# Optimization experiments

Measured on AMD Instinct MI355X. Metric: run time of the kernel, lower is better.

## Reference

```python
import jax, jax.numpy as jnp
import numpy as np

H = 4096
B = 64


def _lstm_cell(x, h, c, W_ih, W_hh, b_ih, b_hh):
    # PyTorch gate order: i, f, g, o. gates: [B, 4H]
    gates = x @ W_ih.T + b_ih + h @ W_hh.T + b_hh
    i, f, g, o = jnp.split(gates, 4, axis=-1)
    c_new = jax.nn.sigmoid(f) * c + jax.nn.sigmoid(i) * jnp.tanh(g)
    h_new = jax.nn.sigmoid(o) * jnp.tanh(c_new)
    return h_new, c_new


def setup_inputs() -> dict:
    key = jax.random.key(0)
    ks = jax.random.split(key, 16)
    s = 0.02
    inp = {
        "current_features": jax.random.normal(ks[0], (B, H), jnp.float32),
        "h0": jax.random.normal(ks[1], (2, B, H), jnp.float32),
        "c0": jax.random.normal(ks[2], (2, B, H), jnp.float32),
        # LSTM layer 0
        "W_ih0": jax.random.normal(ks[3], (4 * H, H), jnp.float32) * s,
        "W_hh0": jax.random.normal(ks[4], (4 * H, H), jnp.float32) * s,
        "b_ih0": jax.random.normal(ks[5], (4 * H,), jnp.float32) * s,
        "b_hh0": jax.random.normal(ks[6], (4 * H,), jnp.float32) * s,
        # LSTM layer 1
        "W_ih1": jax.random.normal(ks[7], (4 * H, H), jnp.float32) * s,
        "W_hh1": jax.random.normal(ks[8], (4 * H, H), jnp.float32) * s,
        "b_ih1": jax.random.normal(ks[9], (4 * H,), jnp.float32) * s,
        "b_hh1": jax.random.normal(ks[10], (4 * H,), jnp.float32) * s,
        # count estimator head
        "Wc1": jax.random.normal(ks[11], (H // 2, H), jnp.float32) * s,
        "bc1": jax.random.normal(ks[12], (H // 2,), jnp.float32) * s,
        "Wc2": jax.random.normal(ks[13], (1, H // 2), jnp.float32) * s,
        "bc2": jax.random.normal(ks[14], (1,), jnp.float32) * s,
    }
    return inp


def reference(current_features, h0, c0,
              W_ih0, W_hh0, b_ih0, b_hh0,
              W_ih1, W_hh1, b_ih1, b_hh1,
              Wc1, bc1, Wc2, bc2):
    # Single-step 2-layer LSTM (seq_len=1; inter-layer dropout inactive in eval)
    h1, c1 = _lstm_cell(current_features, h0[0], c0[0], W_ih0, W_hh0, b_ih0, b_hh0)
    h2, c2 = _lstm_cell(h1, h0[1], c0[1], W_ih1, W_hh1, b_ih1, b_hh1)
    memory_state = h2  # [B, H]
    h_new = jnp.stack([h1, h2], axis=0)  # [2, B, H]
    c_new = jnp.stack([c1, c2], axis=0)
    # count head: Linear -> ReLU -> Linear -> ReLU
    hid = jax.nn.relu(memory_state @ Wc1.T + bc1)
    count_estimate = jax.nn.relu(hid @ Wc2.T + bc2)  # [B, 1]
    return memory_state, (h_new, c_new), count_estimate
```

## Files before the change

kernel.cpp:

```cpp
#include <hip/hip_runtime.h>

#define HD 4096
#define NB 64

typedef __attribute__((ext_vector_type(4))) float f32x4;
typedef __attribute__((ext_vector_type(8))) short bf16x8;
typedef __attribute__((ext_vector_type(4))) short s16x4;

__device__ __forceinline__ short f2bf(float f) {
    unsigned u = __float_as_uint(f);
    u += 0x7fffu + ((u >> 16) & 1u);
    return (short)(u >> 16);
}

__device__ __forceinline__ bf16x8 cvt8(f32x4 lo, f32x4 hi) {
    bf16x8 r;
    r[0] = f2bf(lo[0]); r[1] = f2bf(lo[1]); r[2] = f2bf(lo[2]); r[3] = f2bf(lo[3]);
    r[4] = f2bf(hi[0]); r[5] = f2bf(hi[1]); r[6] = f2bf(hi[2]); r[7] = f2bf(hi[3]);
    return r;
}

__device__ __forceinline__ float sigmoidf_(float x) { return 1.f / (1.f + __expf(-x)); }

__global__ void convert_kernel(const float* __restrict__ X, const float* __restrict__ h0,
                               short* __restrict__ Xbf, short* __restrict__ H0bf)
{
    const int i = blockIdx.x * blockDim.x + threadIdx.x;
    if (i < 65536) {
        f32x4 v = ((const f32x4*)X)[i];
        s16x4 o = { f2bf(v[0]), f2bf(v[1]), f2bf(v[2]), f2bf(v[3]) };
        ((s16x4*)Xbf)[i] = o;
    } else {
        const int j = i - 65536;
        f32x4 v = ((const f32x4*)h0)[j];
        s16x4 o = { f2bf(v[0]), f2bf(v[1]), f2bf(v[2]), f2bf(v[3]) };
        ((s16x4*)H0bf)[j] = o;
    }
}

__global__ __launch_bounds__(256, 1) void lstm_layer_kernel(
    const short* __restrict__ Abf0, const short* __restrict__ Abf1,
    const float* __restrict__ Wih, const float* __restrict__ Whh,
    const float* __restrict__ bih, const float* __restrict__ bhh,
    const float* __restrict__ cprev,
    float* __restrict__ hout, float* __restrict__ cout,
    float* __restrict__ hout2, short* __restrict__ hbf)
{
    const int tid  = threadIdx.x;
    const int lane = tid & 63;
    const int wv   = tid >> 6;
    const int ar   = lane & 15;
    const int kg   = lane >> 4;
    const int hc0  = blockIdx.x * 16;

    const long jrow = (long)wv * HD + hc0 + ar;
    const short* aSrc[2] = { Abf0 + (long)ar * HD + kg * 8, Abf1 + (long)ar * HD + kg * 8 };
    const float* wSrc[2] = { Wih + jrow * HD + kg * 8,      Whh + jrow * HD + kg * 8 };

    const f32x4 zero = {0.f, 0.f, 0.f, 0.f};
    f32x4 acc[4] = {zero, zero, zero, zero};

    for (int s = 0; s < 2; ++s) {
        const short* pa = aSrc[s];
        const float* pw = wSrc[s];
        bf16x8 a[2][4][2];
        f32x4  w[2][2][2];

        #pragma unroll
        for (int m = 0; m < 4; ++m)
            #pragma unroll
            for (int ks = 0; ks < 2; ++ks)
                a[0][m][ks] = *(const bf16x8*)(pa + m * 16 * HD + ks * 32);
        #pragma unroll
        for (int ks = 0; ks < 2; ++ks) {
            w[0][ks][0] = *(const f32x4*)(pw + ks * 32);
            w[0][ks][1] = *(const f32x4*)(pw + ks * 32 + 4);
        }

        #pragma unroll 2
        for (int t = 0; t < 64; ++t) {
            const int cur = t & 1, nxt = cur ^ 1;
            if (t < 63) {
                const int ko = (t + 1) * 64;
                #pragma unroll
                for (int m = 0; m < 4; ++m)
                    #pragma unroll
                    for (int ks = 0; ks < 2; ++ks)
                        a[nxt][m][ks] = *(const bf16x8*)(pa + m * 16 * HD + ko + ks * 32);
                #pragma unroll
                for (int ks = 0; ks < 2; ++ks) {
                    w[nxt][ks][0] = *(const f32x4*)(pw + ko + ks * 32);
                    w[nxt][ks][1] = *(const f32x4*)(pw + ko + ks * 32 + 4);
                }
            }
            #pragma unroll
            for (int ks = 0; ks < 2; ++ks) {
                const bf16x8 wb = cvt8(w[cur][ks][0], w[cur][ks][1]);
                #pragma unroll
                for (int m = 0; m < 4; ++m)
                    acc[m] = __builtin_amdgcn_mfma_f32_16x16x32_bf16(
                                 a[cur][m][ks], wb, acc[m], 0, 0, 0);
            }
        }
    }

    const float bias = bih[wv * HD + hc0 + ar] + bhh[wv * HD + hc0 + ar];

    __shared__ float Sg[4][64][17];
    #pragma unroll
    for (int m = 0; m < 4; ++m)
        #pragma unroll
        for (int r = 0; r < 4; ++r)
            Sg[wv][m * 16 + kg * 4 + r][ar] = acc[m][r] + bias;
    __syncthreads();

    #pragma unroll
    for (int p = 0; p < 4; ++p) {
        const int idx = tid + p * 256;
        const int b = idx >> 4, hc = idx & 15;
        const float ig = Sg[0][b][hc], fg = Sg[1][b][hc];
        const float gg = Sg[2][b][hc], og = Sg[3][b][hc];
        const long off = (long)b * HD + hc0 + hc;
        const float co = cprev[off];
        const float cn = sigmoidf_(fg) * co + sigmoidf_(ig) * tanhf(gg);
        const float hn = sigmoidf_(og) * tanhf(cn);
        hout[off] = hn;
        cout[off] = cn;
        if (hout2) hout2[off] = hn;
        hbf[off] = f2bf(hn);
    }
}

__global__ __launch_bounds__(256, 1) void head_kernel(
    const short* __restrict__ Abf, const float* __restrict__ Wc1,
    const float* __restrict__ bc1, float* __restrict__ hid)
{
    const int tid = threadIdx.x, lane = tid & 63, wv = tid >> 6;
    const int ar = lane & 15, kg = lane >> 4;
    const int n0 = blockIdx.x * 16;

    const short* pa = Abf + (long)ar * HD + wv * 1024 + kg * 8;
    const float* pw = Wc1 + (long)(n0 + ar) * HD + wv * 1024 + kg * 8;

    const f32x4 zero = {0.f, 0.f, 0.f, 0.f};
    f32x4 acc[4] = {zero, zero, zero, zero};
    bf16x8 a[2][4][2];
    f32x4  w[2][2][2];

    #pragma unroll
    for (int m = 0; m < 4; ++m)
        #pragma unroll
        for (int ks = 0; ks < 2; ++ks)
            a[0][m][ks] = *(const bf16x8*)(pa + m * 16 * HD + ks * 32);
    #pragma unroll
    for (int ks = 0; ks < 2; ++ks) {
        w[0][ks][0] = *(const f32x4*)(pw + ks * 32);
        w[0][ks][1] = *(const f32x4*)(pw + ks * 32 + 4);
    }

    #pragma unroll 2
    for (int t = 0; t < 16; ++t) {
        const int cur = t & 1, nxt = cur ^ 1;
        if (t < 15) {
            const int ko = (t + 1) * 64;
            #pragma unroll
            for (int m = 0; m < 4; ++m)
                #pragma unroll
                for (int ks = 0; ks < 2; ++ks)
                    a[nxt][m][ks] = *(const bf16x8*)(pa + m * 16 * HD + ko + ks * 32);
            #pragma unroll
            for (int ks = 0; ks < 2; ++ks) {
                w[nxt][ks][0] = *(const f32x4*)(pw + ko + ks * 32);
                w[nxt][ks][1] = *(const f32x4*)(pw + ko + ks * 32 + 4);
            }
        }
        #pragma unroll
        for (int ks = 0; ks < 2; ++ks) {
            const bf16x8 wb = cvt8(w[cur][ks][0], w[cur][ks][1]);
            #pragma unroll
            for (int m = 0; m < 4; ++m)
                acc[m] = __builtin_amdgcn_mfma_f32_16x16x32_bf16(
                             a[cur][m][ks], wb, acc[m], 0, 0, 0);
        }
    }

    __shared__ float Sg[4][64][17];
    #pragma unroll
    for (int m = 0; m < 4; ++m)
        #pragma unroll
        for (int r = 0; r < 4; ++r)
            Sg[wv][m * 16 + kg * 4 + r][ar] = acc[m][r];
    __syncthreads();

    #pragma unroll
    for (int p = 0; p < 4; ++p) {
        const int idx = tid + p * 256;
        const int b = idx >> 4, hc = idx & 15;
        const float v = Sg[0][b][hc] + Sg[1][b][hc] + Sg[2][b][hc] + Sg[3][b][hc]
                      + bc1[n0 + hc];
        hid[(long)b * 2048 + n0 + hc] = fmaxf(v, 0.f);
    }
}

__global__ void count_kernel(const float* __restrict__ hid, const float* __restrict__ Wc2,
                             const float* __restrict__ bc2, float* __restrict__ out)
{
    const int tid = threadIdx.x;
    const int b = tid >> 2, q = tid & 3;
    const float* hp = hid + (long)b * 2048 + q * 512;
    const float* wp = Wc2 + q * 512;
    float s = 0.f;
    #pragma unroll 4
    for (int k = 0; k < 512; k += 4) {
        f32x4 h4 = *(const f32x4*)(hp + k);
        f32x4 w4 = *(const f32x4*)(wp + k);
        s += h4[0] * w4[0] + h4[1] * w4[1] + h4[2] * w4[2] + h4[3] * w4[3];
    }
    s += __shfl_xor(s, 1);
    s += __shfl_xor(s, 2);
    if (q == 0) out[b] = fmaxf(s + bc2[0], 0.f);
}

extern "C" void kernel_launch(void* const* d_in, const int* in_sizes, int n_in,
                              void* d_out, int out_size, void* d_ws, size_t ws_size,
                              hipStream_t stream)
{
    const float* X    = (const float*)d_in[0];
    const float* h0   = (const float*)d_in[1];
    const float* c0   = (const float*)d_in[2];
    const float* Wih0 = (const float*)d_in[3];
    const float* Whh0 = (const float*)d_in[4];
    const float* bih0 = (const float*)d_in[5];
    const float* bhh0 = (const float*)d_in[6];
    const float* Wih1 = (const float*)d_in[7];
    const float* Whh1 = (const float*)d_in[8];
    const float* bih1 = (const float*)d_in[9];
    const float* bhh1 = (const float*)d_in[10];
    const float* Wc1  = (const float*)d_in[11];
    const float* bc1  = (const float*)d_in[12];
    const float* Wc2  = (const float*)d_in[13];
    const float* bc2  = (const float*)d_in[14];

    float* out  = (float*)d_out;
    float* ms   = out;
    float* hnew = out + 262144;
    float* cnew = out + 786432;
    float* cnt  = out + 1310720;

    char* ws = (char*)d_ws;
    short* Xbf  = (short*)ws;
    short* H0bf = (short*)(ws + 524288);
    short* h1bf = (short*)(ws + 1572864);
    short* h2bf = (short*)(ws + 2097152);
    float* hid  = (float*)(ws + 2621440);

    hipLaunchKernelGGL(convert_kernel, dim3(768), dim3(256), 0, stream, X, h0, Xbf, H0bf);

    hipLaunchKernelGGL(lstm_layer_kernel, dim3(256), dim3(256), 0, stream,
                       Xbf, H0bf, Wih0, Whh0, bih0, bhh0, c0,
                       hnew, cnew, (float*)nullptr, h1bf);

    hipLaunchKernelGGL(lstm_layer_kernel, dim3(256), dim3(256), 0, stream,
                       h1bf, H0bf + 262144, Wih1, Whh1, bih1, bhh1, c0 + 262144,
                       hnew + 262144, cnew + 262144, ms, h2bf);

    hipLaunchKernelGGL(head_kernel, dim3(128), dim3(256), 0, stream, h2bf, Wc1, bc1, hid);
    hipLaunchKernelGGL(count_kernel, dim3(1), dim3(256), 0, stream, hid, Wc2, bc2, cnt);
}
```

Baseline: 413.7 us.

## Split LSTM GEMMs along K into partial sums with LDS-staged weights

Replaces the fused per-layer LSTM kernel and the head kernel with a split-K GEMM that writes partial gate sums to workspace, followed by separate reduction and activation kernels. More blocks can then stream the large fp32 weight matrices concurrently. Weights are loaded asynchronously into swizzled LDS via global_load_lds with explicit waitcnt pipelining, and converted with packed bf16 conversion instructions. The cost is extra partial-sum traffic to workspace, added kernel launches, and a choice of split factor that depends on workspace size.

New measurement: 383.8 us. 7.2% less time.

```diff
diff --git a/kernel.cpp b/kernel.cpp
--- a/kernel.cpp
+++ b/kernel.cpp
@@ -1,7 +1,6 @@
 #include <hip/hip_runtime.h>
 
 #define HD 4096
-#define NB 64
 
 typedef __attribute__((ext_vector_type(4))) float f32x4;
 typedef __attribute__((ext_vector_type(8))) short bf16x8;
@@ -13,11 +12,19 @@
     return (short)(u >> 16);
 }
 
-__device__ __forceinline__ bf16x8 cvt8(f32x4 lo, f32x4 hi) {
-    bf16x8 r;
-    r[0] = f2bf(lo[0]); r[1] = f2bf(lo[1]); r[2] = f2bf(lo[2]); r[3] = f2bf(lo[3]);
-    r[4] = f2bf(hi[0]); r[5] = f2bf(hi[1]); r[6] = f2bf(hi[2]); r[7] = f2bf(hi[3]);
-    return r;
+__device__ __forceinline__ bf16x8 cvt8pk(f32x4 lo, f32x4 hi) {
+    union { bf16x8 v; unsigned u[4]; } r;
+    asm("v_cvt_pk_bf16_f32 %0, %1, %2" : "=v"(r.u[0]) : "v"(lo[0]), "v"(lo[1]));
+    asm("v_cvt_pk_bf16_f32 %0, %1, %2" : "=v"(r.u[1]) : "v"(lo[2]), "v"(lo[3]));
+    asm("v_cvt_pk_bf16_f32 %0, %1, %2" : "=v"(r.u[2]) : "v"(hi[0]), "v"(hi[1]));
+    asm("v_cvt_pk_bf16_f32 %0, %1, %2" : "=v"(r.u[3]) : "v"(hi[2]), "v"(hi[3]));
+    return r.v;
+}
+
+__device__ __forceinline__ void gl_lds16(const float* g, float* l) {
+    typedef const __attribute__((address_space(1))) void* gas_t;
+    typedef __attribute__((address_space(3))) void* las_t;
+    __builtin_amdgcn_global_load_lds((gas_t)(const void*)g, (las_t)(void*)l, 16, 0, 0);
 }
 
 __device__ __forceinline__ float sigmoidf_(float x) { return 1.f / (1.f + __expf(-x)); }
@@ -38,168 +45,135 @@
     }
 }
 
-__global__ __launch_bounds__(256, 1) void lstm_layer_kernel(
-    const short* __restrict__ Abf0, const short* __restrict__ Abf1,
-    const float* __restrict__ Wih, const float* __restrict__ Whh,
-    const float* __restrict__ bih, const float* __restrict__ bhh,
-    const float* __restrict__ cprev,
-    float* __restrict__ hout, float* __restrict__ cout,
-    float* __restrict__ hout2, short* __restrict__ hbf)
-{
-    const int tid  = threadIdx.x;
-    const int lane = tid & 63;
-    const int wv   = tid >> 6;
-    const int ar   = lane & 15;
-    const int kg   = lane >> 4;
-    const int hc0  = blockIdx.x * 16;
-
-    const long jrow = (long)wv * HD + hc0 + ar;
-    const short* aSrc[2] = { Abf0 + (long)ar * HD + kg * 8, Abf1 + (long)ar * HD + kg * 8 };
-    const float* wSrc[2] = { Wih + jrow * HD + kg * 8,      Whh + jrow * HD + kg * 8 };
+#define STAGE(LB, TT) \
+    _Pragma("unroll") for (int i_ = 0; i_ < 4; ++i_) \
+        gl_lds16(wsrc[i_] + (TT) * 64, (LB) + i_ * 256);
+
+#define ALOAD(BUF, TT) \
+    _Pragma("unroll") for (int m_ = 0; m_ < 4; ++m_) \
+    _Pragma("unroll") for (int ks_ = 0; ks_ < 2; ++ks_) \
+        a[BUF][m_][ks_] = *(const bf16x8*)(aBase + m_ * 16 * HD + (TT) * 64 + ks_ * 32);
+
+#define COMP(LB, BUF) \
+    _Pragma("unroll") for (int ks_ = 0; ks_ < 2; ++ks_) { \
+        const int bofs_ = ar * 64 + ks_ * 32; \
+        f32x4 wlo_ = *(const f32x4*)((LB) + bofs_ + ((((kg * 2)    ) ^ (ar & 7)) << 2)); \
+        f32x4 whi_ = *(const f32x4*)((LB) + bofs_ + ((((kg * 2) + 1) ^ (ar & 7)) << 2)); \
+        bf16x8 wb_ = cvt8pk(wlo_, whi_); \
+        _Pragma("unroll") for (int m_ = 0; m_ < 4; ++m_) \
+            acc[m_] = __builtin_amdgcn_mfma_f32_16x16x32_bf16(a[BUF][m_][ks_], wb_, acc[m_], 0, 0, 0); \
+    }
+
+__global__ __launch_bounds__(256, 4) void gemm_part_kernel(
+    const short* __restrict__ A0, const short* __restrict__ A1,
+    const float* __restrict__ W0, const float* __restrict__ W1,
+    float* __restrict__ P, int N, int nkq, int KB)
+{
+    __shared__ float wlds[4][2][1024];
+    const int tid = threadIdx.x, lane = tid & 63, wv = tid >> 6;
+    const int ar = lane & 15, kg = lane >> 4;
+    const int bid = blockIdx.x;
+    const int ntile = bid / nkq, kq = bid % nkq;
+    const int half = nkq >> 1;
+    const int kqh = (kq >= half) ? 1 : 0;
+    const int kqi = kq - kqh * half;
+    const short* A = kqh ? A1 : A0;
+    const float* W = kqh ? W1 : W0;
+    const int kbase = kqi * KB;
+    const int T = KB >> 6;
+    const int n0w = ntile * 64 + wv * 16;
+
+    const short* aBase = A + (long)ar * HD + kbase + kg * 8;
+
+    const float* wsrc[4];
+    #pragma unroll
+    for (int i = 0; i < 4; ++i) {
+        const int row = i * 4 + kg;
+        wsrc[i] = W + (long)(n0w + row) * HD + kbase + (((lane & 15) ^ (row & 7)) << 2);
+    }
+    float* lb0 = &wlds[wv][0][0];
+    float* lb1 = &wlds[wv][1][0];
 
     const f32x4 zero = {0.f, 0.f, 0.f, 0.f};
     f32x4 acc[4] = {zero, zero, zero, zero};
-
-    for (int s = 0; s < 2; ++s) {
-        const short* pa = aSrc[s];
-        const float* pw = wSrc[s];
-        bf16x8 a[2][4][2];
-        f32x4  w[2][2][2];
-
-        #pragma unroll
-        for (int m = 0; m < 4; ++m)
-            #pragma unroll
-            for (int ks = 0; ks < 2; ++ks)
-                a[0][m][ks] = *(const bf16x8*)(pa + m * 16 * HD + ks * 32);
-        #pragma unroll
-        for (int ks = 0; ks < 2; ++ks) {
-            w[0][ks][0] = *(const f32x4*)(pw + ks * 32);
-            w[0][ks][1] = *(const f32x4*)(pw + ks * 32 + 4);
+    bf16x8 a[2][4][2];
+
+    STAGE(lb0, 0); ALOAD(0, 0);
+    const int T2 = T >> 1;
+    for (int u = 0; u < T2; ++u) {
+        const int t0 = u * 2, t1 = t0 + 1;
+        STAGE(lb1, t1); ALOAD(1, t1);
+        asm volatile("s_waitcnt vmcnt(12)" ::: "memory");
+        __builtin_amdgcn_sched_barrier(0);
+        COMP(lb0, 0);
+        if (u + 1 < T2) {
+            STAGE(lb0, t0 + 2); ALOAD(0, t0 + 2);
+            asm volatile("s_waitcnt vmcnt(12)" ::: "memory");
+        } else {
+            asm volatile("s_waitcnt vmcnt(0)" ::: "memory");
         }
-
-        #pragma unroll 2
-        for (int t = 0; t < 64; ++t) {
-            const int cur = t & 1, nxt = cur ^ 1;
-            if (t < 63) {
-                const int ko = (t + 1) * 64;
-                #pragma unroll
-                for (int m = 0; m < 4; ++m)
-                    #pragma unroll
-                    for (int ks = 0; ks < 2; ++ks)
-                        a[nxt][m][ks] = *(const bf16x8*)(pa + m * 16 * HD + ko + ks * 32);
-                #pragma unroll
-                for (int ks = 0; ks < 2; ++ks) {
-                    w[nxt][ks][0] = *(const f32x4*)(pw + ko + ks * 32);
-                    w[nxt][ks][1] = *(const f32x4*)(pw + ko + ks * 32 + 4);
-                }
-            }
-            #pragma unroll
-            for (int ks = 0; ks < 2; ++ks) {
-                const bf16x8 wb = cvt8(w[cur][ks][0], w[cur][ks][1]);
-                #pragma unroll
-                for (int m = 0; m < 4; ++m)
-                    acc[m] = __builtin_amdgcn_mfma_f32_16x16x32_bf16(
-                                 a[cur][m][ks], wb, acc[m], 0, 0, 0);
-            }
-        }
-    }
-
-    const float bias = bih[wv * HD + hc0 + ar] + bhh[wv * HD + hc0 + ar];
-
-    __shared__ float Sg[4][64][17];
+        __builtin_amdgcn_sched_barrier(0);
+        COMP(lb1, 1);
+    }
+
+    float* pr = P + (long)kq * 64 * N + n0w + ar;
     #pragma unroll
     for (int m = 0; m < 4; ++m)
         #pragma unroll
         for (int r = 0; r < 4; ++r)
-            Sg[wv][m * 16 + kg * 4 + r][ar] = acc[m][r] + bias;
-    __syncthreads();
-
-    #pragma unroll
-    for (int p = 0; p < 4; ++p) {
-        const int idx = tid + p * 256;
-        const int b = idx >> 4, hc = idx & 15;
-        const float ig = Sg[0][b][hc], fg = Sg[1][b][hc];
-        const float gg = Sg[2][b][hc], og = Sg[3][b][hc];
-        const long off = (long)b * HD + hc0 + hc;
-        const float co = cprev[off];
-        const float cn = sigmoidf_(fg) * co + sigmoidf_(ig) * tanhf(gg);
-        const float hn = sigmoidf_(og) * tanhf(cn);
-        hout[off] = hn;
-        cout[off] = cn;
-        if (hout2) hout2[off] = hn;
-        hbf[off] = f2bf(hn);
-    }
-}
-
-__global__ __launch_bounds__(256, 1) void head_kernel(
-    const short* __restrict__ Abf, const float* __restrict__ Wc1,
-    const float* __restrict__ bc1, float* __restrict__ hid)
-{
-    const int tid = threadIdx.x, lane = tid & 63, wv = tid >> 6;
-    const int ar = lane & 15, kg = lane >> 4;
-    const int n0 = blockIdx.x * 16;
-
-    const short* pa = Abf + (long)ar * HD + wv * 1024 + kg * 8;
-    const float* pw = Wc1 + (long)(n0 + ar) * HD + wv * 1024 + kg * 8;
-
-    const f32x4 zero = {0.f, 0.f, 0.f, 0.f};
-    f32x4 acc[4] = {zero, zero, zero, zero};
-    bf16x8 a[2][4][2];
-    f32x4  w[2][2][2];
-
-    #pragma unroll
-    for (int m = 0; m < 4; ++m)
+            pr[(long)(m * 16 + kg * 4 + r) * N] = acc[m][r];
+}
+
+__global__ void cell_kernel(const float* __restrict__ P, int nkq,
+                            const float* __restrict__ bi, const float* __restrict__ bh,
+                            const float* __restrict__ cprev,
+                            float* __restrict__ hout, float* __restrict__ cout,
+                            float* __restrict__ ms, short* __restrict__ hbf)
+{
+    const int idx = blockIdx.x * blockDim.x + threadIdx.x;
+    const int b = idx >> 10;
+    const int hc = (idx & 1023) * 4;
+
+    f32x4 g[4] = {{0,0,0,0},{0,0,0,0},{0,0,0,0},{0,0,0,0}};
+    for (int kq = 0; kq < nkq; ++kq) {
+        const float* pb = P + ((long)kq * 64 + b) * 16384 + hc;
         #pragma unroll
-        for (int ks = 0; ks < 2; ++ks)
-            a[0][m][ks] = *(const bf16x8*)(pa + m * 16 * HD + ks * 32);
-    #pragma unroll
-    for (int ks = 0; ks < 2; ++ks) {
-        w[0][ks][0] = *(const f32x4*)(pw + ks * 32);
-        w[0][ks][1] = *(const f32x4*)(pw + ks * 32 + 4);
-    }
-
-    #pragma unroll 2
-    for (int t = 0; t < 16; ++t) {
-        const int cur = t & 1, nxt = cur ^ 1;
-        if (t < 15) {
-            const int ko = (t + 1) * 64;
-            #pragma unroll
-            for (int m = 0; m < 4; ++m)
-                #pragma unroll
-                for (int ks = 0; ks < 2; ++ks)
-                    a[nxt][m][ks] = *(const bf16x8*)(pa + m * 16 * HD + ko + ks * 32);
-            #pragma unroll
-            for (int ks = 0; ks < 2; ++ks) {
-                w[nxt][ks][0] = *(const f32x4*)(pw + ko + ks * 32);
-                w[nxt][ks][1] = *(const f32x4*)(pw + ko + ks * 32 + 4);
-            }
-        }
-        #pragma unroll
-        for (int ks = 0; ks < 2; ++ks) {
-            const bf16x8 wb = cvt8(w[cur][ks][0], w[cur][ks][1]);
-            #pragma unroll
-            for (int m = 0; m < 4; ++m)
-                acc[m] = __builtin_amdgcn_mfma_f32_16x16x32_bf16(
-                             a[cur][m][ks], wb, acc[m], 0, 0, 0);
-        }
-    }
-
-    __shared__ float Sg[4][64][17];
-    #pragma unroll
-    for (int m = 0; m < 4; ++m)
-        #pragma unroll
-        for (int r = 0; r < 4; ++r)
-            Sg[wv][m * 16 + kg * 4 + r][ar] = acc[m][r];
-    __syncthreads();
-
-    #pragma unroll
-    for (int p = 0; p < 4; ++p) {
-        const int idx = tid + p * 256;
-        const int b = idx >> 4, hc = idx & 15;
-        const float v = Sg[0][b][hc] + Sg[1][b][hc] + Sg[2][b][hc] + Sg[3][b][hc]
-                      + bc1[n0 + hc];
-        hid[(long)b * 2048 + n0 + hc] = fmaxf(v, 0.f);
-    }
+        for (int gt = 0; gt < 4; ++gt)
+            g[gt] += *(const f32x4*)(pb + gt * 4096);
+    }
+    #pragma unroll
+    for (int gt = 0; gt < 4; ++gt) {
+        g[gt] += *(const f32x4*)(bi + gt * HD + hc);
+        g[gt] += *(const f32x4*)(bh + gt * HD + hc);
+    }
+    const long off = (long)b * HD + hc;
+    f32x4 c = *(const f32x4*)(cprev + off);
+    f32x4 hn, cn; s16x4 hb;
+    #pragma unroll
+    for (int e = 0; e < 4; ++e) {
+        float cv = sigmoidf_(g[1][e]) * c[e] + sigmoidf_(g[0][e]) * tanhf(g[2][e]);
+        float hv = sigmoidf_(g[3][e]) * tanhf(cv);
+        cn[e] = cv; hn[e] = hv; hb[e] = f2bf(hv);
+    }
+    *(f32x4*)(hout + off) = hn;
+    *(f32x4*)(cout + off) = cn;
+    if (ms) *(f32x4*)(ms + off) = hn;
+    *(s16x4*)(hbf + off) = hb;
+}
+
+__global__ void headfin_kernel(const float* __restrict__ P, int nkq,
+                               const float* __restrict__ bc1, float* __restrict__ hid)
+{
+    const int idx = blockIdx.x * blockDim.x + threadIdx.x;
+    const int b = idx >> 9;
+    const int n = (idx & 511) * 4;
+    f32x4 s = {0.f, 0.f, 0.f, 0.f};
+    for (int kq = 0; kq < nkq; ++kq)
+        s += *(const f32x4*)(P + ((long)kq * 64 + b) * 2048 + n);
+    s += *(const f32x4*)(bc1 + n);
+    #pragma unroll
+    for (int e = 0; e < 4; ++e) s[e] = fmaxf(s[e], 0.f);
+    *(f32x4*)(hid + (long)b * 2048 + n) = s;
 }
 
 __global__ void count_kernel(const float* __restrict__ hid, const float* __restrict__ Wc2,
@@ -249,21 +223,29 @@
 
     char* ws = (char*)d_ws;
     short* Xbf  = (short*)ws;
-    short* H0bf = (short*)(ws + 524288);
-    short* h1bf = (short*)(ws + 1572864);
-    short* h2bf = (short*)(ws + 2097152);
-    float* hid  = (float*)(ws + 2621440);
+    short* H0bf = (short*)(ws + (1u << 19));
+    short* h1bf = (short*)(ws + 3u * (1u << 19));
+    short* h2bf = (short*)(ws + (1u << 21));
+    float* hid  = (float*)(ws + 5u * (1u << 19));
+    float* Pp   = (float*)(ws + 3u * (1u << 20));
+
+    const int nkq = (ws_size >= (3u + 16u) * (1u << 20)) ? 4 : 2;
+    const int KBl = (nkq == 4) ? 2048 : 4096;
 
     hipLaunchKernelGGL(convert_kernel, dim3(768), dim3(256), 0, stream, X, h0, Xbf, H0bf);
 
-    hipLaunchKernelGGL(lstm_layer_kernel, dim3(256), dim3(256), 0, stream,
-                       Xbf, H0bf, Wih0, Whh0, bih0, bhh0, c0,
-                       hnew, cnew, (float*)nullptr, h1bf);
-
-    hipLaunchKernelGGL(lstm_layer_kernel, dim3(256), dim3(256), 0, stream,
-                       h1bf, H0bf + 262144, Wih1, Whh1, bih1, bhh1, c0 + 262144,
-                       hnew + 262144, cnew + 262144, ms, h2bf);
-
-    hipLaunchKernelGGL(head_kernel, dim3(128), dim3(256), 0, stream, h2bf, Wc1, bc1, hid);
+    hipLaunchKernelGGL(gemm_part_kernel, dim3(256 * nkq), dim3(256), 0, stream,
+                       Xbf, H0bf, Wih0, Whh0, Pp, 16384, nkq, KBl);
+    hipLaunchKernelGGL(cell_kernel, dim3(256), dim3(256), 0, stream,
+                       Pp, nkq, bih0, bhh0, c0, hnew, cnew, (float*)nullptr, h1bf);
+
+    hipLaunchKernelGGL(gemm_part_kernel, dim3(256 * nkq), dim3(256), 0, stream,
+                       h1bf, H0bf + 262144, Wih1, Whh1, Pp, 16384, nkq, KBl);
+    hipLaunchKernelGGL(cell_kernel, dim3(256), dim3(256), 0, stream,
+                       Pp, nkq, bih1, bhh1, c0 + 262144, hnew + 262144, cnew + 262144, ms, h2bf);
+
+    hipLaunchKernelGGL(gemm_part_kernel, dim3(32 * 8), dim3(256), 0, stream,
+                       h2bf, h2bf + 2048, Wc1, Wc1 + 2048, Pp, 2048, 8, 512);
+    hipLaunchKernelGGL(headfin_kernel, dim3(128), dim3(256), 0, stream, Pp, 8, bc1, hid);
     hipLaunchKernelGGL(count_kernel, dim3(1), dim3(256), 0, stream, hid, Wc2, bc2, cnt);
 }
```
